# Kernel optimization log

Measured on AMD Instinct MI355X. Metric: run time of the kernel, lower is better.

## Reference

```python
import jax, jax.numpy as jnp
import numpy as np


def setup_inputs() -> dict:
    key = jax.random.key(0)
    x = jax.random.normal(key, (256, 1024), dtype=jnp.float32)
    return {"x": x}


def reference(x):
    # SelMul: for input row [a, b, c] output is [a*a, a*b, a*c, b*b, b*c, c*c],
    # i.e. x[:, i] * x[:, j] for all i <= j, in row-major upper-triangular order.
    # The torch original materializes the full n^2 outer product then slices;
    # here we gather only the n(n+1)/2 needed pairs directly.
    n = x.shape[-1]
    rows, cols = jnp.triu_indices(n)  # rows[k] <= cols[k], row-major order
    return x[:, rows] * x[:, cols]  # (B, n*(n+1)//2)
```

## Files before the change

kernel.cpp:

```cpp
#include <hip/hip_runtime.h>


#define N 1024
#define TRI (N * (N + 1) / 2)

__global__ __launch_bounds__(256) void selmul_kernel(const float* __restrict__ x,
                                                     float* __restrict__ out) {
    const int i = blockIdx.x;
    const int b = blockIdx.y;
    const float* __restrict__ xrow = x + b * N;
    const float xi = xrow[i];

    const int tri_off = i * N - (i * (i - 1)) / 2;
    float* __restrict__ o = out + (size_t)b * TRI + tri_off;
    const int len = N - i;
    const int tid = threadIdx.x;

    int head = (4 - (tri_off & 3)) & 3;
    if (head > len) head = len;
    if (tid < head) o[tid] = xi * xrow[i + tid];

    const int len2 = len - head;
    const int nvec = len2 >> 2;
    const float* __restrict__ xv = xrow + i + head;
    float4* __restrict__ ov = (float4*)(o + head);

    for (int v = tid; v < nvec; v += 256) {
        const int j = v << 2;
        float4 r;
        r.x = xi * xv[j + 0];
        r.y = xi * xv[j + 1];
        r.z = xi * xv[j + 2];
        r.w = xi * xv[j + 3];
        ov[v] = r;
    }

    const int rem = len2 & 3;
    if (tid < rem) {
        const int j = (nvec << 2) + tid;
        o[head + j] = xi * xv[j];
    }
}

extern "C" void kernel_launch(void* const* d_in, const int* in_sizes, int n_in,
                              void* d_out, int out_size, void* d_ws, size_t ws_size,
                              hipStream_t stream) {
    const float* x = (const float*)d_in[0];
    float* out = (float*)d_out;
    const int B = in_sizes[0] / N;
    dim3 grid(N, B);
    selmul_kernel<<<grid, 256, 0, stream>>>(x, out);
}
```

Before: 632.4 us.

## Flatten output into grid-stride float4 loop with triangular index inversion

Replaces the per-(row,batch) block decomposition, where block work shrinks with i and many threads idle, with a flat grid-stride loop over every aligned float4 of the whole output. Each thread recovers (i,j) from its linear triangular offset using a float sqrt with an integer fixup, then walks across row boundaries inside its four elements. This balances load and gives fully aligned vector stores. In exchange it adds per-element index math and scattered gather loads of x.

```diff
diff --git a/kernel.cpp b/kernel.cpp
--- a/kernel.cpp
+++ b/kernel.cpp
@@ -3,42 +3,42 @@
 
 #define N 1024
 #define TRI (N * (N + 1) / 2)
+#define TRI4 (TRI / 4)
+#define TPB 256
+#define NBLOCKS 8192
 
-__global__ __launch_bounds__(256) void selmul_kernel(const float* __restrict__ x,
-                                                     float* __restrict__ out) {
-    const int i = blockIdx.x;
-    const int b = blockIdx.y;
-    const float* __restrict__ xrow = x + b * N;
-    const float xi = xrow[i];
+__global__ __launch_bounds__(TPB) void selmul_kernel(const float* __restrict__ x,
+                                                     float* __restrict__ out,
+                                                     int total4) {
+    const int stride = gridDim.x * TPB;
+    for (int v = blockIdx.x * TPB + threadIdx.x; v < total4; v += stride) {
+        const int b = (int)((unsigned)v / TRI4);
+        const int r = (v - b * TRI4) << 2;
 
-    const int tri_off = i * N - (i * (i - 1)) / 2;
-    float* __restrict__ o = out + (size_t)b * TRI + tri_off;
-    const int len = N - i;
-    const int tid = threadIdx.x;
+        const float s = sqrtf(4198401.0f - 8.0f * (float)r);
+        int i = (int)((2049.0f - s) * 0.5f);
+        int rs = (i * (2049 - i)) >> 1;
+        if (rs > r) {
+            --i;
+            rs = (i * (2049 - i)) >> 1;
+        } else {
+            const int rs1 = ((i + 1) * (2048 - i)) >> 1;
+            if (rs1 <= r) { ++i; rs = rs1; }
+        }
+        int j = i + (r - rs);
 
-    int head = (4 - (tri_off & 3)) & 3;
-    if (head > len) head = len;
-    if (tid < head) o[tid] = xi * xrow[i + tid];
+        const float* __restrict__ xrow = x + b * N;
+        float xi = xrow[i];
+        float4 o;
+        o.x = xi * xrow[j];
+        if (++j >= N) { ++i; j = i; xi = xrow[i]; }
+        o.y = xi * xrow[j];
+        if (++j >= N) { ++i; j = i; xi = xrow[i]; }
+        o.z = xi * xrow[j];
+        if (++j >= N) { ++i; j = i; xi = xrow[i]; }
+        o.w = xi * xrow[j];
 
-    const int len2 = len - head;
-    const int nvec = len2 >> 2;
-    const float* __restrict__ xv = xrow + i + head;
-    float4* __restrict__ ov = (float4*)(o + head);
-
-    for (int v = tid; v < nvec; v += 256) {
-        const int j = v << 2;
-        float4 r;
-        r.x = xi * xv[j + 0];
-        r.y = xi * xv[j + 1];
-        r.z = xi * xv[j + 2];
-        r.w = xi * xv[j + 3];
-        ov[v] = r;
-    }
-
-    const int rem = len2 & 3;
-    if (tid < rem) {
-        const int j = (nvec << 2) + tid;
-        o[head + j] = xi * xv[j];
+        ((float4*)out)[v] = o;
     }
 }
 
@@ -47,7 +47,6 @@
                               hipStream_t stream) {
     const float* x = (const float*)d_in[0];
     float* out = (float*)d_out;
-    const int B = in_sizes[0] / N;
-    dim3 grid(N, B);
-    selmul_kernel<<<grid, 256, 0, stream>>>(x, out);
+    const int total4 = out_size >> 2;
+    selmul_kernel<<<NBLOCKS, TPB, 0, stream>>>(x, out, total4);
 }
```

After: 603.4 us. -4.6%, faster.
